# Optimization experiments

Hardware: AMD Instinct MI355X
Metric: run time of the kernel (lower is better)

## Reference

```python
import jax, jax.numpy as jnp
import numpy as np

N_NODES = 100_000
DEG = 16
N_EDGES = N_NODES * DEG
NODE_F = 128
EDGE_F = 16
HID = 64
B = 64
K = DEG


def setup_inputs() -> dict:
    key = jax.random.key(0)
    ks = jax.random.split(key, 12)
    # node i's outgoing edges are at ids i + k*N_NODES for k in [0, DEG)
    src = jnp.arange(N_EDGES, dtype=jnp.int32) % N_NODES
    dst = jax.random.randint(ks[0], (N_EDGES,), 0, N_NODES, dtype=jnp.int32)
    edge_index = jnp.stack([src, dst])
    current_nodes = jax.random.randint(ks[1], (B,), 0, N_NODES, dtype=jnp.int32)
    # reachable neighbors = destinations of the current node's real edges
    neighbor_nodes = dst[current_nodes[:, None] + jnp.arange(K, dtype=jnp.int32)[None, :] * N_NODES]
    x = jax.random.normal(ks[2], (N_NODES, NODE_F), jnp.float32)
    edge_attr = jax.random.normal(ks[3], (N_EDGES, EDGE_F), jnp.float32)
    return dict(
        x=x,
        edge_attr=edge_attr,
        conv1_W=jax.random.normal(ks[4], (NODE_F, HID), jnp.float32) * (NODE_F ** -0.5),
        conv1_b=jnp.zeros((HID,), jnp.float32),
        conv2_W=jax.random.normal(ks[5], (HID, HID), jnp.float32) * (HID ** -0.5),
        conv2_b=jnp.zeros((HID,), jnp.float32),
        mlp_W1=jax.random.normal(ks[6], (2 * HID + EDGE_F, 2 * HID), jnp.float32) * ((2 * HID + EDGE_F) ** -0.5),
        mlp_b1=jnp.zeros((2 * HID,), jnp.float32),
        mlp_W2=jax.random.normal(ks[7], (2 * HID, 1), jnp.float32) * ((2 * HID) ** -0.5),
        mlp_b2=jnp.zeros((1,), jnp.float32),
        edge_index=edge_index,
        current_nodes=current_nodes,
        neighbor_nodes=neighbor_nodes,
    )


def gcn_conv(x, edge_index, W, b):
    """PyG GCNConv: symmetric norm with self-loops, then linear + bias."""
    n = x.shape[0]
    loop = jnp.arange(n, dtype=edge_index.dtype)
    src = jnp.concatenate([edge_index[0], loop])  # messages flow src -> dst
    dst = jnp.concatenate([edge_index[1], loop])
    xw = x @ W                                    # [N, H]
    deg = jnp.zeros((n,), xw.dtype).at[dst].add(1.0)
    dinv = jnp.where(deg > 0, jax.lax.rsqrt(deg), 0.0)
    msg = (dinv[src] * dinv[dst])[:, None] * xw[src]      # [E+N, H]
    return jax.ops.segment_sum(msg, dst, num_segments=n) + b


def reference(x, edge_attr, conv1_W, conv1_b, conv2_W, conv2_b,
              mlp_W1, mlp_b1, mlp_W2, mlp_b2,
              edge_index, current_nodes, neighbor_nodes):
    n = x.shape[0]
    h = jax.nn.relu(gcn_conv(x, edge_index, conv1_W, conv1_b))
    h = jax.nn.relu(gcn_conv(h, edge_index, conv2_W, conv2_b))

    # First edge id matching each (current, neighbor) pair, replacing the
    # original O(E)-per-neighbor boolean-mask loop with a sorted-key lookup.
    keys = edge_index[0].astype(jnp.int64) * n + edge_index[1].astype(jnp.int64)
    order = jnp.argsort(keys, stable=True)        # stable -> leftmost == first edge id
    skeys = keys[order]
    query = current_nodes[:, None].astype(jnp.int64) * n + neighbor_nodes.astype(jnp.int64)
    pos = jnp.clip(jnp.searchsorted(skeys, query), 0, skeys.shape[0] - 1)
    valid = skeys[pos] == query                   # [B, K]
    eid = order[pos]
    ea = edge_attr[eid]                           # [B, K, F]

    b_, k_ = neighbor_nodes.shape
    h_cur = jnp.broadcast_to(h[current_nodes][:, None, :], (b_, k_, h.shape[1]))
    h_nbr = h[neighbor_nodes]
    m = jnp.concatenate([h_cur, h_nbr, ea], axis=-1)  # [B, K, 2H+F]
    q = (jax.nn.relu(m @ mlp_W1 + mlp_b1) @ mlp_W2 + mlp_b2)[..., 0]
    q = jnp.where(valid, q, 0.0)
    return q, valid
```

## Files before the change

### kernel.cpp

```cpp
#include <hip/hip_runtime.h>

#define N_NODES 100000
#define DEG 16
#define N_EDGES (N_NODES * DEG)
#define NODE_F 128
#define EDGE_F 16
#define HID 64
#define NQ 1024
#define NCHUNK (N_EDGES / 256)
#define NHIST 3125
#define HE (N_EDGES / 2)
#define XT64 ((N_NODES + 63) / 64)
#define TOTAL_A (NHIST + XT64)
#define BMW ((N_NODES + 31) / 32)
#define BCAP 56
#define NDINV ((N_NODES + 255) / 256)

__device__ __forceinline__ int xcc_id() {
  int x;
  asm("s_getreg_b32 %0, hwreg(HW_REG_XCC_ID)" : "=s"(x));
  return x & 7;
}

__device__ __forceinline__ int bm_test(const unsigned* __restrict__ bm, int v) {
  return (bm[v >> 5] >> (v & 31)) & 1u;
}

__global__ __launch_bounds__(1024) void k_query_init(
    const int* __restrict__ dst, const int* __restrict__ cur,
    const int* __restrict__ nbr, unsigned* __restrict__ n1bm,
    unsigned* __restrict__ n2bm, int* __restrict__ wcur,
    int* __restrict__ eid_sel, float* __restrict__ out_valid,
    int* __restrict__ degp) {
  const int t = threadIdx.x;
  if (blockIdx.x > 0) {
    int4* d4 = (int4*)degp;
    const int n4 = 8 * N_NODES / 4;
    int i = (blockIdx.x - 1) * 1024 + t;
    const int stride = (gridDim.x - 1) * 1024;
    for (; i < n4; i += stride) d4[i] = make_int4(0, 0, 0, 0);
    return;
  }
  __shared__ unsigned lbm[2 * BMW];
  for (int i = t; i < 2 * BMW; i += 1024) lbm[i] = 0u;
  __syncthreads();
  int b = t >> 4;
  int c = cur[b];
  int nb = nbr[t];
  int sel = -1;
  #pragma unroll
  for (int j = 0; j < DEG; ++j) {
    int e = c + j * N_NODES;
    if (sel < 0 && dst[e] == nb) sel = e;
  }
  eid_sel[t] = sel;
  out_valid[t] = (sel >= 0) ? 1.0f : 0.0f;
  atomicOr(&lbm[c >> 5],        1u << (c & 31));
  atomicOr(&lbm[nb >> 5],       1u << (nb & 31));
  atomicOr(&lbm[BMW + (c >> 5)],  1u << (c & 31));
  atomicOr(&lbm[BMW + (nb >> 5)], 1u << (nb & 31));
  wcur[c] = 0;  wcur[nb] = 0;
  __syncthreads();
  for (int i = t; i < BMW; i += 1024) {
    n1bm[i] = lbm[i];
    n2bm[i] = lbm[BMW + i];
  }
}

__global__ __launch_bounds__(256) void k_fusedA(
    const float* __restrict__ x, const float* __restrict__ Wg,
    float* __restrict__ xw, const int* __restrict__ dst,
    const unsigned* __restrict__ n2bm, unsigned* __restrict__ n1bm,
    int* __restrict__ wcur, int* __restrict__ degp) {
  __shared__ float4 xs4[64 * 16];
  const int t = threadIdx.x;
  const int bid = blockIdx.x;

  if (bid < NHIST) {
    int* __restrict__ dp = degp + (size_t)xcc_id() * N_NODES;
    int e0 = bid * 256 + t;
    int d0 = dst[e0];
    int d1 = dst[e0 + HE];
    __hip_atomic_fetch_add(&dp[d0], 1, __ATOMIC_RELAXED,
                           __HIP_MEMORY_SCOPE_WORKGROUP);
    __hip_atomic_fetch_add(&dp[d1], 1, __ATOMIC_RELAXED,
                           __HIP_MEMORY_SCOPE_WORKGROUP);
    unsigned w0 = n2bm[d0 >> 5];
    unsigned w1 = n2bm[d1 >> 5];
    bool m0 = (w0 >> (d0 & 31)) & 1u;
    bool m1 = (w1 >> (d1 & 31)) & 1u;
    if (m0 | m1) {
      int s = e0 % N_NODES;
      __hip_atomic_fetch_or(&n1bm[s >> 5], 1u << (s & 31), __ATOMIC_RELAXED,
                            __HIP_MEMORY_SCOPE_AGENT);
      wcur[s] = 0;
    }
    return;
  }

  const long base = (long)(bid - NHIST) * 64;
  const float4* __restrict__ xv = (const float4*)x;
  const int rg = (t >> 4) << 2;
  const int cq = t & 15;
  const float4* __restrict__ wq = (const float4*)Wg + cq;
  const int sw = (rg >> 2) & 7;

  float acc[4][4];
  #pragma unroll
  for (int i = 0; i < 4; ++i)
    #pragma unroll
    for (int j = 0; j < 4; ++j) acc[i][j] = 0.f;

  #pragma unroll
  for (int half = 0; half < 2; ++half) {
    #pragma unroll
    for (int p = 0; p < 4; ++p) {
      int f4 = p * 256 + t;
      int r = f4 >> 4;
      int kk = f4 & 15;
      long gr = base + r;
      float4 v = (gr < N_NODES) ? xv[gr * 32 + half * 16 + kk]
                                : make_float4(0.f, 0.f, 0.f, 0.f);
      xs4[r * 16 + (kk ^ ((r >> 2) & 7))] = v;
    }
    __syncthreads();
    for (int kk = 0; kk < 16; ++kk) {
      int k4 = half * 16 + kk;
      float4 xf0 = xs4[(rg + 0) * 16 + (kk ^ sw)];
      float4 xf1 = xs4[(rg + 1) * 16 + (kk ^ sw)];
      float4 xf2 = xs4[(rg + 2) * 16 + (kk ^ sw)];
      float4 xf3 = xs4[(rg + 3) * 16 + (kk ^ sw)];
      float4 wf0 = wq[(k4 * 4 + 0) * 16];
      float4 wf1 = wq[(k4 * 4 + 1) * 16];
      float4 wf2 = wq[(k4 * 4 + 2) * 16];
      float4 wf3 = wq[(k4 * 4 + 3) * 16];
#define FMA_ROW(i, xf)                                                  \
      acc[i][0] = fmaf(xf.x, wf0.x, acc[i][0]);                         \
      acc[i][1] = fmaf(xf.x, wf0.y, acc[i][1]);                         \
      acc[i][2] = fmaf(xf.x, wf0.z, acc[i][2]);                         \
      acc[i][3] = fmaf(xf.x, wf0.w, acc[i][3]);                         \
      acc[i][0] = fmaf(xf.y, wf1.x, acc[i][0]);                         \
      acc[i][1] = fmaf(xf.y, wf1.y, acc[i][1]);                         \
      acc[i][2] = fmaf(xf.y, wf1.z, acc[i][2]);                         \
      acc[i][3] = fmaf(xf.y, wf1.w, acc[i][3]);                         \
      acc[i][0] = fmaf(xf.z, wf2.x, acc[i][0]);                         \
      acc[i][1] = fmaf(xf.z, wf2.y, acc[i][1]);                         \
      acc[i][2] = fmaf(xf.z, wf2.z, acc[i][2]);                         \
      acc[i][3] = fmaf(xf.z, wf2.w, acc[i][3]);                         \
      acc[i][0] = fmaf(xf.w, wf3.x, acc[i][0]);                         \
      acc[i][1] = fmaf(xf.w, wf3.y, acc[i][1]);                         \
      acc[i][2] = fmaf(xf.w, wf3.z, acc[i][2]);                         \
      acc[i][3] = fmaf(xf.w, wf3.w, acc[i][3]);
      FMA_ROW(0, xf0)
      FMA_ROW(1, xf1)
      FMA_ROW(2, xf2)
      FMA_ROW(3, xf3)
#undef FMA_ROW
    }
    __syncthreads();
  }

  #pragma unroll
  for (int i = 0; i < 4; ++i) {
    long gr = base + rg + i;
    if (gr < N_NODES) {
      float4* __restrict__ op = (float4*)(xw + gr * HID);
      op[cq] = make_float4(acc[i][0], acc[i][1], acc[i][2], acc[i][3]);
    }
  }
}

__global__ void k_bucket_dinv(const int* __restrict__ dst,
                              const unsigned* __restrict__ n1bm,
                              int* __restrict__ wcur, int* __restrict__ bucket,
                              const int* __restrict__ degp, float* __restrict__ dinv) {
  if (blockIdx.x < NDINV) {
    int v = blockIdx.x * 256 + threadIdx.x;
    if (v < N_NODES) {
      int s = 1;
      #pragma unroll
      for (int p = 0; p < 8; ++p) s += degp[(size_t)p * N_NODES + v];
      dinv[v] = rsqrtf((float)s);
    }
    return;
  }
  int e = (blockIdx.x - NDINV) * 256 + threadIdx.x;
  int d = dst[e];
  if (!bm_test(n1bm, d)) return;
  int pos = atomicAdd(&wcur[d], 1);
  if (pos >= 0 && pos < BCAP)
    bucket[(size_t)d * BCAP + pos] = e % N_NODES;
}

__global__ __launch_bounds__(256) void k_gather_xw2(
    const int* __restrict__ bucket, const int* __restrict__ wcur,
    const unsigned* __restrict__ n1bm, const float* __restrict__ dinv,
    const float* __restrict__ xw, const float* __restrict__ bias,
    const float* __restrict__ W2g, float* __restrict__ xw2) {
  const int t = threadIdx.x;
  const int lane = t & 63;
  const int v = blockIdx.x * 4 + (t >> 6);
  if (v >= N_NODES) return;
  if (!bm_test(n1bm, v)) return;
  int n = wcur[v];
  if (n > BCAP) n = BCAP;
  if (n < 0) n = 0;
  int   s_l = (lane < n) ? bucket[(size_t)v * BCAP + lane] : 0;
  float w_l = (lane < n) ? dinv[s_l] : 0.f;
  float acc = 0.f;
  int j = 0;
  for (; j + 3 < n; j += 4) {
    int s0 = __shfl(s_l, j);
    int s1 = __shfl(s_l, j + 1);
    int s2 = __shfl(s_l, j + 2);
    int s3 = __shfl(s_l, j + 3);
    float a0 = xw[(size_t)s0 * HID + lane];
    float a1 = xw[(size_t)s1 * HID + lane];
    float a2 = xw[(size_t)s2 * HID + lane];
    float a3 = xw[(size_t)s3 * HID + lane];
    acc = fmaf(__shfl(w_l, j), a0, acc);
    acc = fmaf(__shfl(w_l, j + 1), a1, acc);
    acc = fmaf(__shfl(w_l, j + 2), a2, acc);
    acc = fmaf(__shfl(w_l, j + 3), a3, acc);
  }
  for (; j < n; ++j)
    acc = fmaf(__shfl(w_l, j), xw[(size_t)__shfl(s_l, j) * HID + lane], acc);
  float dv = dinv[v];
  acc = fmaf(dv, xw[(size_t)v * HID + lane], acc);
  float h = fmaxf(fmaf(dv, acc, bias[lane]), 0.f);
  float a2s = 0.f;
  #pragma unroll
  for (int f = 0; f < HID; ++f)
    a2s = fmaf(__shfl(h, f), W2g[f * HID + lane], a2s);
  xw2[(size_t)v * HID + lane] = a2s;
}

__global__ __launch_bounds__(256) void k_gather(
    const int* __restrict__ bucket, const int* __restrict__ wcur,
    const unsigned* __restrict__ fbm, const float* __restrict__ dinv,
    const float* __restrict__ xw, const float* __restrict__ bias,
    float* __restrict__ hout) {
  const int t = threadIdx.x;
  const int lane = t & 63;
  const int v = blockIdx.x * 4 + (t >> 6);
  if (v >= N_NODES) return;
  if (!bm_test(fbm, v)) return;
  int n = wcur[v];
  if (n > BCAP) n = BCAP;
  if (n < 0) n = 0;
  int   s_l = (lane < n) ? bucket[(size_t)v * BCAP + lane] : 0;
  float w_l = (lane < n) ? dinv[s_l] : 0.f;
  float acc = 0.f;
  int j = 0;
  for (; j + 3 < n; j += 4) {
    int s0 = __shfl(s_l, j);
    int s1 = __shfl(s_l, j + 1);
    int s2 = __shfl(s_l, j + 2);
    int s3 = __shfl(s_l, j + 3);
    float a0 = xw[(size_t)s0 * HID + lane];
    float a1 = xw[(size_t)s1 * HID + lane];
    float a2 = xw[(size_t)s2 * HID + lane];
    float a3 = xw[(size_t)s3 * HID + lane];
    acc = fmaf(__shfl(w_l, j), a0, acc);
    acc = fmaf(__shfl(w_l, j + 1), a1, acc);
    acc = fmaf(__shfl(w_l, j + 2), a2, acc);
    acc = fmaf(__shfl(w_l, j + 3), a3, acc);
  }
  for (; j < n; ++j)
    acc = fmaf(__shfl(w_l, j), xw[(size_t)__shfl(s_l, j) * HID + lane], acc);
  float dv = dinv[v];
  acc = fmaf(dv, xw[(size_t)v * HID + lane], acc);
  hout[(size_t)v * HID + lane] = fmaxf(fmaf(dv, acc, bias[lane]), 0.f);
}

__global__ void k_mlp(const float* __restrict__ h2, const float* __restrict__ ea,
                      const float* __restrict__ W1, const float* __restrict__ b1,
                      const float* __restrict__ W2, const float* __restrict__ b2,
                      const int* __restrict__ cur, const int* __restrict__ nbr,
                      const int* __restrict__ eid_sel, float* __restrict__ out) {
  __shared__ float m[2 * HID + EDGE_F];
  __shared__ float red[128];
  const int q = blockIdx.x;
  const int t = threadIdx.x;
  const int eid = eid_sel[q];
  if (eid < 0) {
    if (t == 0) out[q] = 0.0f;
    return;
  }
  const int b = q >> 4;
  const int c = cur[b];
  const int nb = nbr[q];
  if (t < HID)    m[t] = h2[(size_t)c * HID + t];
  else            m[t] = h2[(size_t)nb * HID + (t - HID)];
  if (t < EDGE_F) m[2 * HID + t] = ea[(size_t)eid * EDGE_F + t];
  __syncthreads();
  float h = b1[t];
  #pragma unroll
  for (int j = 0; j < 2 * HID + EDGE_F; ++j) h = fmaf(m[j], W1[j * 128 + t], h);
  h = fmaxf(h, 0.f) * W2[t];
  red[t] = h;
  __syncthreads();
  if (t < 64) {
    float v = red[t] + red[t + 64];
    #pragma unroll
    for (int o = 32; o > 0; o >>= 1) v += __shfl_down(v, o);
    if (t == 0) out[q] = v + b2[0];
  }
}

extern "C" void kernel_launch(void* const* d_in, const int* in_sizes, int n_in,
                              void* d_out, int out_size, void* d_ws, size_t ws_size,
                              hipStream_t stream) {
  const float* x    = (const float*)d_in[0];
  const float* ea   = (const float*)d_in[1];
  const float* c1W  = (const float*)d_in[2];
  const float* c1b  = (const float*)d_in[3];
  const float* c2W  = (const float*)d_in[4];
  const float* c2b  = (const float*)d_in[5];
  const float* mW1  = (const float*)d_in[6];
  const float* mb1  = (const float*)d_in[7];
  const float* mW2  = (const float*)d_in[8];
  const float* mb2  = (const float*)d_in[9];
  const int*   eidx = (const int*)d_in[10];
  const int*   cur  = (const int*)d_in[11];
  const int*   nbr  = (const int*)d_in[12];
  const int* edst = eidx + N_EDGES;
  float* out = (float*)d_out;

  char* p = (char*)d_ws;
  auto alloc = [&](size_t bytes) -> void* {
    void* r = (void*)p;
    p += (bytes + 255) & ~(size_t)255;
    return r;
  };
  int*      degp    = (int*)alloc((size_t)8 * N_NODES * 4);
  float*    dinv    = (float*)alloc((size_t)N_NODES * 4);
  unsigned* n1bm    = (unsigned*)alloc((size_t)BMW * 4);
  unsigned* n2bm    = (unsigned*)alloc((size_t)BMW * 4);
  int*      wcur    = (int*)alloc((size_t)N_NODES * 4);
  int*      eid_sel = (int*)alloc((size_t)NQ * 4);
  int*      bucket  = (int*)alloc((size_t)N_NODES * BCAP * 4);
  float*    xw1     = (float*)alloc((size_t)N_NODES * HID * 4);
  float*    xw2     = (float*)alloc((size_t)N_NODES * HID * 4);
  float*    h2      = xw1;

  k_query_init<<<65, 1024, 0, stream>>>(edst, cur, nbr, n1bm, n2bm, wcur,
                                        eid_sel, out + NQ, degp);
  k_fusedA<<<TOTAL_A, 256, 0, stream>>>(x, c1W, xw1, edst, n2bm, n1bm, wcur,
                                        degp);
  k_bucket_dinv<<<NDINV + NCHUNK, 256, 0, stream>>>(edst, n1bm, wcur, bucket,
                                                    degp, dinv);
  k_gather_xw2<<<(N_NODES + 3) / 4, 256, 0, stream>>>(bucket, wcur, n1bm, dinv,
                                                      xw1, c1b, c2W, xw2);
  k_gather<<<(N_NODES + 3) / 4, 256, 0, stream>>>(bucket, wcur, n2bm, dinv, xw2,
                                                  c2b, h2);
  k_mlp<<<NQ, 128, 0, stream>>>(h2, ea, mW1, mb1, mW2, mb2, cur, nbr, eid_sel, out);
}
```

Before: 352.4 us.

## Split fused histogram/GEMM kernel and software-pipeline the GEMM weight loads

Splits the combined degree-histogram and x@W kernel into two separate launches. The histogram now reads dst as int2 (two adjacent edges per thread) instead of two strided halves. The GEMM stages the full 64x128 x tile in shared memory at once, dropping the second barrier pair, and double-buffers the weight register loads across k-steps. This adds a kernel launch and loses the overlap between histogram and GEMM blocks, and it doubles LDS per block, which may lower occupancy.

```diff
diff --git a/kernel.cpp b/kernel.cpp
--- a/kernel.cpp
+++ b/kernel.cpp
@@ -8,10 +8,8 @@
 #define HID 64
 #define NQ 1024
 #define NCHUNK (N_EDGES / 256)
-#define NHIST 3125
-#define HE (N_EDGES / 2)
+#define NH2 (N_EDGES / 512)
 #define XT64 ((N_NODES + 63) / 64)
-#define TOTAL_A (NHIST + XT64)
 #define BMW ((N_NODES + 31) / 32)
 #define BCAP 56
 #define NDINV ((N_NODES + 255) / 256)
@@ -67,39 +65,52 @@
   }
 }
 
-__global__ __launch_bounds__(256) void k_fusedA(
+__global__ __launch_bounds__(256) void k_hist(
+    const int* __restrict__ dst, const unsigned* __restrict__ n2bm,
+    unsigned* __restrict__ n1bm, int* __restrict__ wcur,
+    int* __restrict__ degp) {
+  int i = blockIdx.x * 256 + threadIdx.x;
+  int2 d = ((const int2*)dst)[i];
+  int* __restrict__ dp = degp + (size_t)xcc_id() * N_NODES;
+  __hip_atomic_fetch_add(&dp[d.x], 1, __ATOMIC_RELAXED,
+                         __HIP_MEMORY_SCOPE_WORKGROUP);
+  __hip_atomic_fetch_add(&dp[d.y], 1, __ATOMIC_RELAXED,
+                         __HIP_MEMORY_SCOPE_WORKGROUP);
+  int e0 = 2 * i;
+  if (bm_test(n2bm, d.x)) {
+    int s = e0 % N_NODES;
+    __hip_atomic_fetch_or(&n1bm[s >> 5], 1u << (s & 31), __ATOMIC_RELAXED,
+                          __HIP_MEMORY_SCOPE_AGENT);
+    wcur[s] = 0;
+  }
+  if (bm_test(n2bm, d.y)) {
+    int s = (e0 + 1) % N_NODES;
+    __hip_atomic_fetch_or(&n1bm[s >> 5], 1u << (s & 31), __ATOMIC_RELAXED,
+                          __HIP_MEMORY_SCOPE_AGENT);
+    wcur[s] = 0;
+  }
+}
+
+__global__ __launch_bounds__(256) void k_gemm(
     const float* __restrict__ x, const float* __restrict__ Wg,
-    float* __restrict__ xw, const int* __restrict__ dst,
-    const unsigned* __restrict__ n2bm, unsigned* __restrict__ n1bm,
-    int* __restrict__ wcur, int* __restrict__ degp) {
-  __shared__ float4 xs4[64 * 16];
-  const int t = threadIdx.x;
-  const int bid = blockIdx.x;
-
-  if (bid < NHIST) {
-    int* __restrict__ dp = degp + (size_t)xcc_id() * N_NODES;
-    int e0 = bid * 256 + t;
-    int d0 = dst[e0];
-    int d1 = dst[e0 + HE];
-    __hip_atomic_fetch_add(&dp[d0], 1, __ATOMIC_RELAXED,
-                           __HIP_MEMORY_SCOPE_WORKGROUP);
-    __hip_atomic_fetch_add(&dp[d1], 1, __ATOMIC_RELAXED,
-                           __HIP_MEMORY_SCOPE_WORKGROUP);
-    unsigned w0 = n2bm[d0 >> 5];
-    unsigned w1 = n2bm[d1 >> 5];
-    bool m0 = (w0 >> (d0 & 31)) & 1u;
-    bool m1 = (w1 >> (d1 & 31)) & 1u;
-    if (m0 | m1) {
-      int s = e0 % N_NODES;
-      __hip_atomic_fetch_or(&n1bm[s >> 5], 1u << (s & 31), __ATOMIC_RELAXED,
-                            __HIP_MEMORY_SCOPE_AGENT);
-      wcur[s] = 0;
-    }
-    return;
-  }
-
-  const long base = (long)(bid - NHIST) * 64;
+    float* __restrict__ xw) {
+  __shared__ float4 xs4[64 * 32];
+  const int t = threadIdx.x;
+  const long base = (long)blockIdx.x * 64;
+
   const float4* __restrict__ xv = (const float4*)x;
+  #pragma unroll
+  for (int p = 0; p < 8; ++p) {
+    int f4 = p * 256 + t;
+    int r = f4 >> 5;
+    int k4 = f4 & 31;
+    long gr = base + r;
+    float4 v = (gr < N_NODES) ? xv[gr * 32 + k4]
+                              : make_float4(0.f, 0.f, 0.f, 0.f);
+    xs4[r * 32 + (k4 ^ ((r >> 2) & 7))] = v;
+  }
+  __syncthreads();
+
   const int rg = (t >> 4) << 2;
   const int cq = t & 15;
   const float4* __restrict__ wq = (const float4*)Wg + cq;
@@ -111,54 +122,54 @@
     #pragma unroll
     for (int j = 0; j < 4; ++j) acc[i][j] = 0.f;
 
-  #pragma unroll
-  for (int half = 0; half < 2; ++half) {
-    #pragma unroll
-    for (int p = 0; p < 4; ++p) {
-      int f4 = p * 256 + t;
-      int r = f4 >> 4;
-      int kk = f4 & 15;
-      long gr = base + r;
-      float4 v = (gr < N_NODES) ? xv[gr * 32 + half * 16 + kk]
-                                : make_float4(0.f, 0.f, 0.f, 0.f);
-      xs4[r * 16 + (kk ^ ((r >> 2) & 7))] = v;
-    }
-    __syncthreads();
-    for (int kk = 0; kk < 16; ++kk) {
-      int k4 = half * 16 + kk;
-      float4 xf0 = xs4[(rg + 0) * 16 + (kk ^ sw)];
-      float4 xf1 = xs4[(rg + 1) * 16 + (kk ^ sw)];
-      float4 xf2 = xs4[(rg + 2) * 16 + (kk ^ sw)];
-      float4 xf3 = xs4[(rg + 3) * 16 + (kk ^ sw)];
-      float4 wf0 = wq[(k4 * 4 + 0) * 16];
-      float4 wf1 = wq[(k4 * 4 + 1) * 16];
-      float4 wf2 = wq[(k4 * 4 + 2) * 16];
-      float4 wf3 = wq[(k4 * 4 + 3) * 16];
-#define FMA_ROW(i, xf)                                                  \
-      acc[i][0] = fmaf(xf.x, wf0.x, acc[i][0]);                         \
-      acc[i][1] = fmaf(xf.x, wf0.y, acc[i][1]);                         \
-      acc[i][2] = fmaf(xf.x, wf0.z, acc[i][2]);                         \
-      acc[i][3] = fmaf(xf.x, wf0.w, acc[i][3]);                         \
-      acc[i][0] = fmaf(xf.y, wf1.x, acc[i][0]);                         \
-      acc[i][1] = fmaf(xf.y, wf1.y, acc[i][1]);                         \
-      acc[i][2] = fmaf(xf.y, wf1.z, acc[i][2]);                         \
-      acc[i][3] = fmaf(xf.y, wf1.w, acc[i][3]);                         \
-      acc[i][0] = fmaf(xf.z, wf2.x, acc[i][0]);                         \
-      acc[i][1] = fmaf(xf.z, wf2.y, acc[i][1]);                         \
-      acc[i][2] = fmaf(xf.z, wf2.z, acc[i][2]);                         \
-      acc[i][3] = fmaf(xf.z, wf2.w, acc[i][3]);                         \
-      acc[i][0] = fmaf(xf.w, wf3.x, acc[i][0]);                         \
-      acc[i][1] = fmaf(xf.w, wf3.y, acc[i][1]);                         \
-      acc[i][2] = fmaf(xf.w, wf3.z, acc[i][2]);                         \
-      acc[i][3] = fmaf(xf.w, wf3.w, acc[i][3]);
-      FMA_ROW(0, xf0)
-      FMA_ROW(1, xf1)
-      FMA_ROW(2, xf2)
-      FMA_ROW(3, xf3)
+#define FMA_ROW(i, xf, w0, w1, w2, w3)                                  \
+    acc[i][0] = fmaf(xf.x, w0.x, acc[i][0]);                            \
+    acc[i][1] = fmaf(xf.x, w0.y, acc[i][1]);                            \
+    acc[i][2] = fmaf(xf.x, w0.z, acc[i][2]);                            \
+    acc[i][3] = fmaf(xf.x, w0.w, acc[i][3]);                            \
+    acc[i][0] = fmaf(xf.y, w1.x, acc[i][0]);                            \
+    acc[i][1] = fmaf(xf.y, w1.y, acc[i][1]);                            \
+    acc[i][2] = fmaf(xf.y, w1.z, acc[i][2]);                            \
+    acc[i][3] = fmaf(xf.y, w1.w, acc[i][3]);                            \
+    acc[i][0] = fmaf(xf.z, w2.x, acc[i][0]);                            \
+    acc[i][1] = fmaf(xf.z, w2.y, acc[i][1]);                            \
+    acc[i][2] = fmaf(xf.z, w2.z, acc[i][2]);                            \
+    acc[i][3] = fmaf(xf.z, w2.w, acc[i][3]);                            \
+    acc[i][0] = fmaf(xf.w, w3.x, acc[i][0]);                            \
+    acc[i][1] = fmaf(xf.w, w3.y, acc[i][1]);                            \
+    acc[i][2] = fmaf(xf.w, w3.z, acc[i][2]);                            \
+    acc[i][3] = fmaf(xf.w, w3.w, acc[i][3]);
+
+  float4 wa0 = wq[0 * 16], wa1 = wq[1 * 16], wa2 = wq[2 * 16], wa3 = wq[3 * 16];
+  for (int k4 = 0; k4 < 32; k4 += 2) {
+    float4 wb0 = wq[((k4 + 1) * 4 + 0) * 16];
+    float4 wb1 = wq[((k4 + 1) * 4 + 1) * 16];
+    float4 wb2 = wq[((k4 + 1) * 4 + 2) * 16];
+    float4 wb3 = wq[((k4 + 1) * 4 + 3) * 16];
+    float4 xe0 = xs4[(rg + 0) * 32 + (k4 ^ sw)];
+    float4 xe1 = xs4[(rg + 1) * 32 + (k4 ^ sw)];
+    float4 xe2 = xs4[(rg + 2) * 32 + (k4 ^ sw)];
+    float4 xe3 = xs4[(rg + 3) * 32 + (k4 ^ sw)];
+    FMA_ROW(0, xe0, wa0, wa1, wa2, wa3)
+    FMA_ROW(1, xe1, wa0, wa1, wa2, wa3)
+    FMA_ROW(2, xe2, wa0, wa1, wa2, wa3)
+    FMA_ROW(3, xe3, wa0, wa1, wa2, wa3)
+    int kn = (k4 + 2 < 32) ? k4 + 2 : 0;
+    wa0 = wq[(kn * 4 + 0) * 16];
+    wa1 = wq[(kn * 4 + 1) * 16];
+    wa2 = wq[(kn * 4 + 2) * 16];
+    wa3 = wq[(kn * 4 + 3) * 16];
+    int ko = (k4 + 1) ^ sw;
+    float4 xo0 = xs4[(rg + 0) * 32 + ko];
+    float4 xo1 = xs4[(rg + 1) * 32 + ko];
+    float4 xo2 = xs4[(rg + 2) * 32 + ko];
+    float4 xo3 = xs4[(rg + 3) * 32 + ko];
+    FMA_ROW(0, xo0, wb0, wb1, wb2, wb3)
+    FMA_ROW(1, xo1, wb0, wb1, wb2, wb3)
+    FMA_ROW(2, xo2, wb0, wb1, wb2, wb3)
+    FMA_ROW(3, xo3, wb0, wb1, wb2, wb3)
+  }
 #undef FMA_ROW
-    }
-    __syncthreads();
-  }
 
   #pragma unroll
   for (int i = 0; i < 4; ++i) {
@@ -346,8 +357,8 @@
 
   k_query_init<<<65, 1024, 0, stream>>>(edst, cur, nbr, n1bm, n2bm, wcur,
                                         eid_sel, out + NQ, degp);
-  k_fusedA<<<TOTAL_A, 256, 0, stream>>>(x, c1W, xw1, edst, n2bm, n1bm, wcur,
-                                        degp);
+  k_hist<<<NH2, 256, 0, stream>>>(edst, n2bm, n1bm, wcur, degp);
+  k_gemm<<<XT64, 256, 0, stream>>>(x, c1W, xw1);
   k_bucket_dinv<<<NDINV + NCHUNK, 256, 0, stream>>>(edst, n1bm, wcur, bucket,
                                                     degp, dinv);
   k_gather_xw2<<<(N_NODES + 3) / 4, 256, 0, stream>>>(bucket, wcur, n1bm, dinv,
```

After: 355.1 us. No clear change (+0.8%).
